# Optimization experiments

Hardware: AMD Instinct MI355X
Metric: run time of the kernel (lower is better)

## Reference

```python
import jax, jax.numpy as jnp
import numpy as np

CONF_THRES = 0.25
IOU_THRES = 0.45
TOP_K = 1024          # fixed candidate pool per image (jit-friendly padded NMS)
B, N, C = 64, 25200, 16  # yolov5-face: 3*(80^2+40^2+20^2)=25200 anchors, 16 channels
IMG = 640.0


def setup_inputs() -> dict:
    key = jax.random.key(0)
    k1, k2, k3, k4, k5 = jax.random.split(key, 5)
    cxcy = jax.random.uniform(k1, (B, N, 2)) * (IMG - 32.0) + 16.0   # box centers
    wh = jax.random.uniform(k2, (B, N, 2)) * 120.0 + 8.0             # box sizes
    obj = jax.random.uniform(k3, (B, N, 1))                           # objectness
    lm = jax.random.uniform(k4, (B, N, 10)) * IMG                     # 5 landmarks
    cls = jax.random.uniform(k5, (B, N, 1))                           # face class conf
    x = jnp.concatenate([cxcy, wh, obj, lm, cls], axis=-1)            # [B, N, 16]
    return {"x": x}


def _xywh2xyxy(b):
    cx, cy, w, h = b[..., 0], b[..., 1], b[..., 2], b[..., 3]
    return jnp.stack([cx - w * 0.5, cy - h * 0.5, cx + w * 0.5, cy + h * 0.5], axis=-1)


def _pairwise_iou(boxes):
    # boxes: [K, 4] xyxy -> iou: [K, K]
    x1, y1, x2, y2 = boxes[:, 0], boxes[:, 1], boxes[:, 2], boxes[:, 3]
    area = jnp.clip(x2 - x1, 0.0) * jnp.clip(y2 - y1, 0.0)            # [K]
    ix1 = jnp.maximum(x1[:, None], x1[None, :])
    iy1 = jnp.maximum(y1[:, None], y1[None, :])
    ix2 = jnp.minimum(x2[:, None], x2[None, :])
    iy2 = jnp.minimum(y2[:, None], y2[None, :])
    inter = jnp.clip(ix2 - ix1, 0.0) * jnp.clip(iy2 - iy1, 0.0)
    union = area[:, None] + area[None, :] - inter
    return inter / (union + 1e-9)


def _nms_image(pred):
    # pred: [N, 16] = xywh, obj, 10 landmark coords, cls
    score = pred[:, 4] * pred[:, 15]                                   # obj * cls conf
    s = jnp.where(score > CONF_THRES, score, -1.0)                     # conf filter
    top_s, order = jax.lax.top_k(s, TOP_K)                             # sort desc
    valid = top_s > 0.0
    boxes = _xywh2xyxy(pred[order, :4])                                # [K, 4]
    lm = pred[order, 5:15]                                             # [K, 10]
    iou = _pairwise_iou(boxes)                                         # [K, K]
    idx = jnp.arange(TOP_K)

    def body(i, keep):
        # suppress lower-scored boxes overlapping kept box i
        sup = (iou[i] > IOU_THRES) & (idx > i) & keep[i]
        return keep & ~sup

    keep = jax.lax.fori_loop(0, TOP_K, body, valid)
    conf = jnp.where(valid, top_s, 0.0)[:, None]
    cls_id = jnp.zeros((TOP_K, 1), dtype=pred.dtype)                   # single class: face
    dets = jnp.concatenate([boxes, conf, lm, cls_id], axis=-1)         # [K, 16]
    return dets * keep[:, None].astype(dets.dtype)                     # zero suppressed rows


def reference(x):
    # x: [B, N, 16] -> padded detections [B, TOP_K, 16]
    return jax.vmap(_nms_image)(x)
```

## Files before the change

kernel.cpp:

```cpp
#include <hip/hip_runtime.h>
#include <stdint.h>

#define NBOX 25200
#define NCH  16
#define TOPK 1024
#define NTH  1024
#define NBUCK 4096
#define CAP  2048
#define LISTCAP 12288
#define K1_SLICES 16
#define K1_TH 256
#define ROWS_PER_SLICE (NBOX / K1_SLICES)
#define K1_ITERS 7

#define M45 ((double)0.45f + 0x1p-26)

#define OFF_KEYS  256
#define OFF_BOXES (OFF_KEYS + 64 * LISTCAP * 8)
#define OFF_MASKS (OFF_BOXES + 64 * TOPK * 16)

__device__ __forceinline__ unsigned long long make_key(float p, uint32_t r) {
  return ((unsigned long long)__float_as_uint(p) << 32) |
         (unsigned long long)(0xFFFFFFFFu - r);
}

__device__ __forceinline__ uint32_t bucket_of(uint32_t bits) {
  uint32_t bk = (bits - 0x3E800001u) >> 12;
  return bk > (NBUCK - 1u) ? (NBUCK - 1u) : bk;
}

__global__ __launch_bounds__(K1_TH) void score_kernel(const float* __restrict__ x,
                                                      unsigned long long* __restrict__ keys,
                                                      uint32_t* __restrict__ cnts) {
  const int img = blockIdx.x >> 4;
  const int slice = blockIdx.x & (K1_SLICES - 1);
  const int t = threadIdx.x;
  const int lane = t & 63;
  const float* __restrict__ xb = x + (size_t)img * NBOX * NCH;
  unsigned long long* __restrict__ kl = keys + (size_t)img * LISTCAP;
  const int row0 = slice * ROWS_PER_SLICE;

  float p[K1_ITERS];
  uint32_t mask = 0;
#pragma unroll
  for (int j = 0; j < K1_ITERS; ++j) {
    const int rr = t + j * K1_TH;
    float v = 0.0f;
    if (rr < ROWS_PER_SLICE) {
      const size_t ro = (size_t)(row0 + rr) * NCH;
      v = xb[ro + 4] * xb[ro + 15];
      if (v > 0.25f) mask |= (1u << j);
    }
    p[j] = v;
  }

  const int cntl = __popc(mask);
  uint32_t inc = (uint32_t)cntl;
#pragma unroll
  for (int off = 1; off < 64; off <<= 1) {
    const uint32_t o = __shfl_up(inc, off);
    if (lane >= off) inc += o;
  }
  const uint32_t wtotal = __shfl(inc, 63);
  uint32_t base = 0;
  if (lane == 63 && wtotal) base = atomicAdd(&cnts[img], wtotal);
  base = (uint32_t)__shfl((int)base, 63);

  uint32_t pos = base + (inc - (uint32_t)cntl);
#pragma unroll
  for (int j = 0; j < K1_ITERS; ++j) {
    if ((mask >> j) & 1u) {
      if (pos < LISTCAP)
        kl[pos] = make_key(p[j], (uint32_t)(row0 + t + j * K1_TH));
      ++pos;
    }
  }
}

__global__ __launch_bounds__(NTH, 1) void select_kernel(const float* __restrict__ x,
                                                        const unsigned long long* __restrict__ keys,
                                                        const uint32_t* __restrict__ cnts,
                                                        float* __restrict__ out,
                                                        float4* __restrict__ boxes) {
  __shared__ uint32_t s_hist[NBUCK];
  __shared__ uint32_t s_pos[NBUCK];
  __shared__ unsigned long long s_sorted[CAP];
  __shared__ unsigned long long s_final[TOPK];
  __shared__ uint32_t s_wsum[16];
  __shared__ int s_cut;

  const int t = threadIdx.x;
  const int b = blockIdx.x;
  const int lane = t & 63;
  const int wid = t >> 6;
  const float* __restrict__ xb = x + (size_t)b * NBOX * NCH;
  const unsigned long long* __restrict__ kl = keys + (size_t)b * LISTCAP;
  int cnt = (int)cnts[b];
  if (cnt > LISTCAP) cnt = LISTCAP;

#pragma unroll
  for (int j = 0; j < NBUCK / NTH; ++j) s_hist[t + j * NTH] = 0u;
  s_final[t] = 0ull;
  if (t == 0) s_cut = 0;
  __syncthreads();
  for (int j = t; j < cnt; j += NTH)
    atomicAdd(&s_hist[bucket_of((uint32_t)(kl[j] >> 32))], 1u);
  __syncthreads();

  const uint32_t h0 = s_hist[4 * t], h1 = s_hist[4 * t + 1];
  const uint32_t h2 = s_hist[4 * t + 2], h3 = s_hist[4 * t + 3];
  const uint32_t qs = h0 + h1 + h2 + h3;
  uint32_t v = qs;
#pragma unroll
  for (int off = 1; off < 64; off <<= 1) {
    const uint32_t o = __shfl_down(v, off);
    if (lane + off < 64) v += o;
  }
  if (lane == 0) s_wsum[wid] = v;
  __syncthreads();
  uint32_t tail = 0;
#pragma unroll
  for (int w = 0; w < 16; ++w) if (w > wid) tail += s_wsum[w];
  const uint32_t after = (v - qs) + tail;
  const uint32_t e3 = after, e2 = after + h3, e1 = e2 + h2, e0 = e1 + h1;
  s_pos[4 * t] = e0; s_pos[4 * t + 1] = e1;
  s_pos[4 * t + 2] = e2; s_pos[4 * t + 3] = e3;
  int cand = -1;
  if (e3 + h3 >= TOPK) cand = 4 * t + 3;
  else if (e2 + h2 >= TOPK) cand = 4 * t + 2;
  else if (e1 + h1 >= TOPK) cand = 4 * t + 1;
  else if (e0 + h0 >= TOPK) cand = 4 * t;
  if (cand >= 0) atomicMax(&s_cut, cand);
  __syncthreads();
  const int cut = s_cut;
  int M = (int)(s_pos[cut] + s_hist[cut]);
  if (M > CAP) M = CAP;
  __syncthreads();

  for (int j = t; j < cnt; j += NTH) {
    const unsigned long long key = kl[j];
    const uint32_t bk = bucket_of((uint32_t)(key >> 32));
    if ((int)bk >= cut) {
      const uint32_t pos = atomicAdd(&s_pos[bk], 1u);
      if (pos < CAP) s_sorted[pos] = key;
    }
  }
  __syncthreads();

  for (int p = t; p < M; p += NTH) {
    const unsigned long long key = s_sorted[p];
    const uint32_t bk = bucket_of((uint32_t)(key >> 32));
    int end = (int)s_pos[bk]; if (end > M) end = M;
    int start = end - (int)s_hist[bk]; if (start < 0) start = 0;
    int lr = 0;
    for (int q = start; q < end; ++q) lr += (int)(s_sorted[q] > key);
    const int fp = start + lr;
    if (fp < TOPK) s_final[fp] = key;
  }
  __syncthreads();

  const unsigned long long mykey = s_final[t];
  const uint32_t sbits = (uint32_t)(mykey >> 32);
  const int src = (int)(0xFFFFFFFFu - (uint32_t)(mykey & 0xFFFFFFFFull));
  const bool valid = (sbits != 0u);
  const float conf = valid ? __uint_as_float(sbits) : 0.0f;

  float x1 = 0.f, y1 = 0.f, x2 = 0.f, y2 = 0.f;
  float lm0=0.f,lm1=0.f,lm2=0.f,lm3=0.f,lm4=0.f,lm5=0.f,lm6=0.f,lm7=0.f,lm8=0.f,lm9=0.f;
  if (valid) {
    const float4* rp = (const float4*)(xb + (size_t)src * NCH);
    const float4 q0 = rp[0], q1 = rp[1], q2 = rp[2], q3 = rp[3];
    x1 = q0.x - q0.z * 0.5f;
    y1 = q0.y - q0.w * 0.5f;
    x2 = q0.x + q0.z * 0.5f;
    y2 = q0.y + q0.w * 0.5f;
    lm0 = q1.y; lm1 = q1.z; lm2 = q1.w;
    lm3 = q2.x; lm4 = q2.y; lm5 = q2.z; lm6 = q2.w;
    lm7 = q3.x; lm8 = q3.y; lm9 = q3.z;
  }
  boxes[(size_t)b * TOPK + t] = make_float4(x1, y1, x2, y2);
  float4* op = (float4*)(out + ((size_t)b * TOPK + (size_t)t) * NCH);
  op[0] = make_float4(x1, y1, x2, y2);
  op[1] = make_float4(conf, lm0, lm1, lm2);
  op[2] = make_float4(lm3, lm4, lm5, lm6);
  op[3] = make_float4(lm7, lm8, lm9, 0.0f);
}

__global__ __launch_bounds__(256) void mask_kernel(const float4* __restrict__ boxes,
                                                   unsigned long long* __restrict__ masks) {
  const int img = blockIdx.x / 40;
  const int s = blockIdx.x % 40;
  int rt, wg;
  if (s < 4)        { rt = s;                wg = 0; }
  else if (s < 12)  { rt = 4 + ((s - 4) >> 1);  wg = (s - 4) & 1; }
  else if (s < 24)  { rt = 8 + (s - 12) / 3;    wg = (s - 12) % 3; }
  else              { rt = 12 + ((s - 24) >> 2); wg = (s - 24) & 3; }

  const int t = threadIdx.x;
  const int lane = t & 63;
  const int jw = wg * 4 + (t >> 6);

  __shared__ float4 s_rbox[64];
  if (t < 64) s_rbox[t] = boxes[(size_t)img * TOPK + rt * 64 + t];
  __syncthreads();
  if (jw > rt) return;

  const float4 cb = boxes[(size_t)img * TOPK + jw * 64 + lane];
  const float ca = fmaxf(cb.z - cb.x, 0.f) * fmaxf(cb.w - cb.y, 0.f);

  unsigned long long myword = 0ull;
  for (int rl = 0; rl < 64; ++rl) {
    const float4 rb = s_rbox[rl];
    const float ra = fmaxf(rb.z - rb.x, 0.f) * fmaxf(rb.w - rb.y, 0.f);
    const float iw = fmaxf(fminf(cb.z, rb.z) - fmaxf(cb.x, rb.x), 0.f);
    const float ih = fmaxf(fminf(cb.w, rb.w) - fmaxf(cb.y, rb.y), 0.f);
    const float inter = iw * ih;
    const float den = ((ca + ra) - inter) + 1e-9f;
    const bool sup = (double)inter > M45 * (double)den;
    unsigned long long bal = __ballot(sup);
    if (jw == rt) bal &= ((1ull << rl) - 1ull);
    if (lane == rl) myword = bal;
  }
  masks[((size_t)img * 16 + jw) * TOPK + rt * 64 + lane] = myword;
}

__global__ __launch_bounds__(NTH, 1) void greedy_kernel(const unsigned long long* __restrict__ masks,
                                                        float* __restrict__ out) {
  __shared__ unsigned long long s_alive[16];
  const int t = threadIdx.x;
  const int b = blockIdx.x;
  const int lane = t & 63;
  const int wid = t >> 6;

  const unsigned long long diag = masks[((size_t)b * 16 + wid) * TOPK + t];

  bool keep = true;
  unsigned long long acc = 0ull;

  for (int tile = 0; tile < 16; ++tile) {
    unsigned long long mw = 0ull;
    if (wid > tile) mw = masks[((size_t)b * 16 + tile) * TOPK + t];

    if (wid == tile) {
      if (acc) keep = false;
      unsigned long long vm = __ballot(diag != 0ull);
      while (vm) {
        const int vv = __ffsll((long long)vm) - 1;
        vm &= vm - 1ull;
        const unsigned long long alive = __ballot(keep);
        if (lane == vv && (alive & diag)) keep = false;
      }
      const unsigned long long fin = __ballot(keep);
      if (lane == 0) s_alive[tile] = fin;
    }
    __syncthreads();
    if (wid > tile) acc |= mw & s_alive[tile];
  }

  if (!keep) {
    float4* op = (float4*)(out + ((size_t)b * TOPK + (size_t)t) * NCH);
    const float4 z = make_float4(0.f, 0.f, 0.f, 0.f);
    op[0] = z; op[1] = z; op[2] = z; op[3] = z;
  }
}

extern "C" void kernel_launch(void* const* d_in, const int* in_sizes, int n_in,
                              void* d_out, int out_size, void* d_ws, size_t ws_size,
                              hipStream_t stream) {
  const float* x = (const float*)d_in[0];
  float* out = (float*)d_out;
  uint32_t* cnts = (uint32_t*)d_ws;
  unsigned long long* keys = (unsigned long long*)((char*)d_ws + OFF_KEYS);
  float4* boxes = (float4*)((char*)d_ws + OFF_BOXES);
  unsigned long long* masks = (unsigned long long*)((char*)d_ws + OFF_MASKS);

  hipMemsetAsync(d_ws, 0, 256, stream);
  score_kernel<<<dim3(64 * K1_SLICES), dim3(K1_TH), 0, stream>>>(x, keys, cnts);
  select_kernel<<<dim3(64), dim3(NTH), 0, stream>>>(x, keys, cnts, out, boxes);
  mask_kernel<<<dim3(64 * 40), dim3(256), 0, stream>>>(boxes, masks);
  greedy_kernel<<<dim3(64), dim3(NTH), 0, stream>>>(masks, out);
}
```

Measured before the change: 222.0 us.

## Replace global atomic key list with per-slice segments and drop memset

The score kernel now writes candidate keys into a fixed per-(image, slice) segment, using a block-local prefix over wave totals instead of a global atomicAdd. It stores the per-slice count directly, which removes the workspace memset launch. The select kernel reads the 16 segments, and its bucket-cut search now reduces within each wave before issuing a shared atomic. The mask kernel precomputes row-box areas in shared memory. Together these aim to cut launch overhead and atomic contention, at the cost of a looped 16-segment read pattern in the select kernel.

Result: faster. 206.6 us (-6.9%).

```diff
diff --git a/kernel.cpp b/kernel.cpp
--- a/kernel.cpp
+++ b/kernel.cpp
@@ -7,16 +7,16 @@
 #define NTH  1024
 #define NBUCK 4096
 #define CAP  2048
-#define LISTCAP 12288
 #define K1_SLICES 16
 #define K1_TH 256
 #define ROWS_PER_SLICE (NBOX / K1_SLICES)
 #define K1_ITERS 7
+#define SEGCAP 1600
 
 #define M45 ((double)0.45f + 0x1p-26)
 
-#define OFF_KEYS  256
-#define OFF_BOXES (OFF_KEYS + 64 * LISTCAP * 8)
+#define OFF_KEYS  4096
+#define OFF_BOXES (OFF_KEYS + 64 * K1_SLICES * SEGCAP * 8)
 #define OFF_MASKS (OFF_BOXES + 64 * TOPK * 16)
 
 __device__ __forceinline__ unsigned long long make_key(float p, uint32_t r) {
@@ -36,22 +36,29 @@
   const int slice = blockIdx.x & (K1_SLICES - 1);
   const int t = threadIdx.x;
   const int lane = t & 63;
+  const int wid = t >> 6;
   const float* __restrict__ xb = x + (size_t)img * NBOX * NCH;
-  unsigned long long* __restrict__ kl = keys + (size_t)img * LISTCAP;
+  unsigned long long* __restrict__ kl = keys + ((size_t)img * K1_SLICES + slice) * SEGCAP;
   const int row0 = slice * ROWS_PER_SLICE;
 
   float p[K1_ITERS];
   uint32_t mask = 0;
 #pragma unroll
-  for (int j = 0; j < K1_ITERS; ++j) {
-    const int rr = t + j * K1_TH;
+  for (int j = 0; j < K1_ITERS - 1; ++j) {
+    const size_t ro = (size_t)(row0 + t + j * K1_TH) * NCH;
+    const float v = xb[ro + 4] * xb[ro + 15];
+    if (v > 0.25f) mask |= (1u << j);
+    p[j] = v;
+  }
+  {
+    const int rr = t + (K1_ITERS - 1) * K1_TH;
     float v = 0.0f;
     if (rr < ROWS_PER_SLICE) {
       const size_t ro = (size_t)(row0 + rr) * NCH;
       v = xb[ro + 4] * xb[ro + 15];
-      if (v > 0.25f) mask |= (1u << j);
+      if (v > 0.25f) mask |= (1u << (K1_ITERS - 1));
     }
-    p[j] = v;
+    p[K1_ITERS - 1] = v;
   }
 
   const int cntl = __popc(mask);
@@ -62,19 +69,24 @@
     if (lane >= off) inc += o;
   }
   const uint32_t wtotal = __shfl(inc, 63);
+
+  __shared__ uint32_t s_wtot[4];
+  if (lane == 63) s_wtot[wid] = wtotal;
+  __syncthreads();
   uint32_t base = 0;
-  if (lane == 63 && wtotal) base = atomicAdd(&cnts[img], wtotal);
-  base = (uint32_t)__shfl((int)base, 63);
+#pragma unroll
+  for (int w = 0; w < 4; ++w) if (w < wid) base += s_wtot[w];
 
   uint32_t pos = base + (inc - (uint32_t)cntl);
 #pragma unroll
   for (int j = 0; j < K1_ITERS; ++j) {
     if ((mask >> j) & 1u) {
-      if (pos < LISTCAP)
-        kl[pos] = make_key(p[j], (uint32_t)(row0 + t + j * K1_TH));
+      kl[pos] = make_key(p[j], (uint32_t)(row0 + t + j * K1_TH));
       ++pos;
     }
   }
+  if (t == K1_TH - 1)
+    cnts[img * K1_SLICES + slice] = base + wtotal;
 }
 
 __global__ __launch_bounds__(NTH, 1) void select_kernel(const float* __restrict__ x,
@@ -87,6 +99,7 @@
   __shared__ unsigned long long s_sorted[CAP];
   __shared__ unsigned long long s_final[TOPK];
   __shared__ uint32_t s_wsum[16];
+  __shared__ uint32_t s_cnt16[K1_SLICES];
   __shared__ int s_cut;
 
   const int t = threadIdx.x;
@@ -94,17 +107,24 @@
   const int lane = t & 63;
   const int wid = t >> 6;
   const float* __restrict__ xb = x + (size_t)b * NBOX * NCH;
-  const unsigned long long* __restrict__ kl = keys + (size_t)b * LISTCAP;
-  int cnt = (int)cnts[b];
-  if (cnt > LISTCAP) cnt = LISTCAP;
+  const unsigned long long* __restrict__ kb0 = keys + (size_t)b * K1_SLICES * SEGCAP;
 
 #pragma unroll
   for (int j = 0; j < NBUCK / NTH; ++j) s_hist[t + j * NTH] = 0u;
   s_final[t] = 0ull;
+  if (t < K1_SLICES) {
+    uint32_t c = cnts[b * K1_SLICES + t];
+    s_cnt16[t] = (c > SEGCAP) ? SEGCAP : c;
+  }
   if (t == 0) s_cut = 0;
   __syncthreads();
-  for (int j = t; j < cnt; j += NTH)
-    atomicAdd(&s_hist[bucket_of((uint32_t)(kl[j] >> 32))], 1u);
+#pragma unroll
+  for (int s = 0; s < K1_SLICES; ++s) {
+    const int cs_ = (int)s_cnt16[s];
+    const unsigned long long* seg = kb0 + (size_t)s * SEGCAP;
+    for (int j = t; j < cs_; j += NTH)
+      atomicAdd(&s_hist[bucket_of((uint32_t)(seg[j] >> 32))], 1u);
+  }
   __syncthreads();
 
   const uint32_t h0 = s_hist[4 * t], h1 = s_hist[4 * t + 1];
@@ -130,19 +150,30 @@
   else if (e2 + h2 >= TOPK) cand = 4 * t + 2;
   else if (e1 + h1 >= TOPK) cand = 4 * t + 1;
   else if (e0 + h0 >= TOPK) cand = 4 * t;
-  if (cand >= 0) atomicMax(&s_cut, cand);
+  int wmax = cand;
+#pragma unroll
+  for (int off = 32; off > 0; off >>= 1) {
+    const int o = __shfl_down(wmax, off);
+    if (o > wmax) wmax = o;
+  }
+  if (lane == 0 && wmax >= 0) atomicMax(&s_cut, wmax);
   __syncthreads();
   const int cut = s_cut;
   int M = (int)(s_pos[cut] + s_hist[cut]);
   if (M > CAP) M = CAP;
   __syncthreads();
 
-  for (int j = t; j < cnt; j += NTH) {
-    const unsigned long long key = kl[j];
-    const uint32_t bk = bucket_of((uint32_t)(key >> 32));
-    if ((int)bk >= cut) {
-      const uint32_t pos = atomicAdd(&s_pos[bk], 1u);
-      if (pos < CAP) s_sorted[pos] = key;
+#pragma unroll
+  for (int s = 0; s < K1_SLICES; ++s) {
+    const int cs_ = (int)s_cnt16[s];
+    const unsigned long long* seg = kb0 + (size_t)s * SEGCAP;
+    for (int j = t; j < cs_; j += NTH) {
+      const unsigned long long key = seg[j];
+      const uint32_t bk = bucket_of((uint32_t)(key >> 32));
+      if ((int)bk >= cut) {
+        const uint32_t pos = atomicAdd(&s_pos[bk], 1u);
+        if (pos < CAP) s_sorted[pos] = key;
+      }
     }
   }
   __syncthreads();
@@ -201,7 +232,12 @@
   const int jw = wg * 4 + (t >> 6);
 
   __shared__ float4 s_rbox[64];
-  if (t < 64) s_rbox[t] = boxes[(size_t)img * TOPK + rt * 64 + t];
+  __shared__ float s_rarea[64];
+  if (t < 64) {
+    const float4 rb = boxes[(size_t)img * TOPK + rt * 64 + t];
+    s_rbox[t] = rb;
+    s_rarea[t] = fmaxf(rb.z - rb.x, 0.f) * fmaxf(rb.w - rb.y, 0.f);
+  }
   __syncthreads();
   if (jw > rt) return;
 
@@ -211,7 +247,7 @@
   unsigned long long myword = 0ull;
   for (int rl = 0; rl < 64; ++rl) {
     const float4 rb = s_rbox[rl];
-    const float ra = fmaxf(rb.z - rb.x, 0.f) * fmaxf(rb.w - rb.y, 0.f);
+    const float ra = s_rarea[rl];
     const float iw = fmaxf(fminf(cb.z, rb.z) - fmaxf(cb.x, rb.x), 0.f);
     const float ih = fmaxf(fminf(cb.w, rb.w) - fmaxf(cb.y, rb.y), 0.f);
     const float inter = iw * ih;
@@ -274,7 +310,6 @@
   float4* boxes = (float4*)((char*)d_ws + OFF_BOXES);
   unsigned long long* masks = (unsigned long long*)((char*)d_ws + OFF_MASKS);
 
-  hipMemsetAsync(d_ws, 0, 256, stream);
   score_kernel<<<dim3(64 * K1_SLICES), dim3(K1_TH), 0, stream>>>(x, keys, cnts);
   select_kernel<<<dim3(64), dim3(NTH), 0, stream>>>(x, keys, cnts, out, boxes);
   mask_kernel<<<dim3(64 * 40), dim3(256), 0, stream>>>(boxes, masks);
```
